# Kernel tuning notes

Hardware: AMD Instinct MI355X
Metric: run time of the kernel (lower is better)

## Reference

```python
import jax, jax.numpy as jnp
import numpy as np

L, D_MODEL, D_INNER, D_STATE, D_CONV, DT_RANK, NUM_ORDERS = 16384, 192, 384, 16, 4, 12, 2
NUM_BLOCKS = 2 * NUM_ORDERS
EPS = 1e-5


def rmsnorm(x, w):
    return x * jax.lax.rsqrt(jnp.mean(x * x, axis=-1, keepdims=True) + EPS) * w


def layernorm(x, w, b):
    m = jnp.mean(x, axis=-1, keepdims=True)
    v = jnp.mean((x - m) ** 2, axis=-1, keepdims=True)
    return (x - m) * jax.lax.rsqrt(v + EPS) * w + b


def causal_dw_conv(x, w, b):
    # x: [L, d], w: [d, K] causal depthwise conv (small fixed K loop)
    K = w.shape[1]
    xp = jnp.pad(x, ((K - 1, 0), (0, 0)))
    y = b
    for k in range(K):
        y = y + xp[k:k + x.shape[0]] * w[:, k]
    return y


def selective_scan(u, dt, A, B, C, Dskip):
    # u, dt: [L, d]; A: [d, n]; B, C: [L, n]; Dskip: [d]
    def step(h, inp):
        u_t, dt_t, B_t, C_t = inp
        dA = jnp.exp(dt_t[:, None] * A)                    # [d, n]
        h = dA * h + (dt_t * u_t)[:, None] * B_t[None, :]  # [d, n]
        return h, h @ C_t                                  # y_t: [d]
    h0 = jnp.zeros(A.shape, u.dtype)
    _, ys = jax.lax.scan(step, h0, (u, dt, B, C))
    return ys + u * Dskip


def mamba_block(x, nw, Wi, cw, cb, Wx, Wdt, bdt, A_log, Dp, Wo):
    # pre-RMSNorm residual Mamba block (create_block semantics)
    res = x
    h = rmsnorm(x, nw)
    xz = h @ Wi                              # [L, 2*d_inner]
    xc, z = jnp.split(xz, 2, axis=-1)
    xc = jax.nn.silu(causal_dw_conv(xc, cw, cb))
    proj = xc @ Wx                           # [L, dt_rank + 2*d_state]
    dt_raw = proj[:, :DT_RANK]
    B = proj[:, DT_RANK:DT_RANK + D_STATE]
    C = proj[:, DT_RANK + D_STATE:]
    dt = jax.nn.softplus(dt_raw @ Wdt + bdt)
    y = selective_scan(xc, dt, -jnp.exp(A_log), B, C, Dp)
    y = y * jax.nn.silu(z)
    return res + y @ Wo


def setup_inputs() -> dict:
    key = jax.random.key(0)
    ks = jax.random.split(key, 10)
    s = 0.02
    x = jax.random.normal(ks[0], (L, D_MODEL), jnp.float32)
    orders = jnp.stack([
        jax.random.permutation(jax.random.fold_in(ks[1], o), L)
        for o in range(NUM_ORDERS)
    ]).astype(jnp.int32)                                     # [NUM_ORDERS, L]
    norm_w = jnp.ones((NUM_BLOCKS, D_MODEL), jnp.float32)
    in_proj_w = jax.random.normal(ks[2], (NUM_BLOCKS, D_MODEL, 2 * D_INNER), jnp.float32) * s
    conv_w = jax.random.normal(ks[3], (NUM_BLOCKS, D_INNER, D_CONV), jnp.float32) * s
    conv_b = jnp.zeros((NUM_BLOCKS, D_INNER), jnp.float32)
    x_proj_w = jax.random.normal(ks[4], (NUM_BLOCKS, D_INNER, DT_RANK + 2 * D_STATE), jnp.float32) * s
    dt_w = jax.random.normal(ks[5], (NUM_BLOCKS, DT_RANK, D_INNER), jnp.float32) * s
    dt_b = jnp.full((NUM_BLOCKS, D_INNER), np.log(np.expm1(0.01)), jnp.float32)  # softplus^-1(0.01)
    A_log = jnp.log(jnp.broadcast_to(jnp.arange(1, D_STATE + 1, dtype=jnp.float32),
                                     (NUM_BLOCKS, D_INNER, D_STATE)))
    D_p = jnp.ones((NUM_BLOCKS, D_INNER), jnp.float32)
    out_proj_w = jax.random.normal(ks[6], (NUM_BLOCKS, D_INNER, D_MODEL), jnp.float32) * s
    fwd_ln_w = jnp.ones((NUM_ORDERS, D_MODEL), jnp.float32)
    fwd_ln_b = jnp.zeros((NUM_ORDERS, D_MODEL), jnp.float32)
    bwd_ln_w = jnp.ones((NUM_ORDERS, D_MODEL), jnp.float32)
    bwd_ln_b = jnp.zeros((NUM_ORDERS, D_MODEL), jnp.float32)
    out_ln_w = jnp.ones((NUM_ORDERS, D_MODEL), jnp.float32)
    out_ln_b = jnp.zeros((NUM_ORDERS, D_MODEL), jnp.float32)
    return {"x": x, "orders": orders, "norm_w": norm_w, "in_proj_w": in_proj_w,
            "conv_w": conv_w, "conv_b": conv_b, "x_proj_w": x_proj_w,
            "dt_w": dt_w, "dt_b": dt_b, "A_log": A_log, "D_p": D_p,
            "out_proj_w": out_proj_w, "fwd_ln_w": fwd_ln_w, "fwd_ln_b": fwd_ln_b,
            "bwd_ln_w": bwd_ln_w, "bwd_ln_b": bwd_ln_b,
            "out_ln_w": out_ln_w, "out_ln_b": out_ln_b}


def reference(x, orders, norm_w, in_proj_w, conv_w, conv_b, x_proj_w, dt_w, dt_b,
              A_log, D_p, out_proj_w, fwd_ln_w, fwd_ln_b, bwd_ln_w, bwd_ln_b,
              out_ln_w, out_ln_b):
    out = x
    for o in range(NUM_ORDERS):          # small fixed loop over serialization orders
        idx = orders[o]
        xo = x[idx]                      # serialize voxel tokens in this order
        fb, bb = o, NUM_ORDERS + o       # forward / backward block indices
        f = mamba_block(xo, norm_w[fb], in_proj_w[fb], conv_w[fb], conv_b[fb],
                        x_proj_w[fb], dt_w[fb], dt_b[fb], A_log[fb], D_p[fb], out_proj_w[fb])
        b = mamba_block(xo[::-1], norm_w[bb], in_proj_w[bb], conv_w[bb], conv_b[bb],
                        x_proj_w[bb], dt_w[bb], dt_b[bb], A_log[bb], D_p[bb], out_proj_w[bb])[::-1]
        comb = layernorm(f, fwd_ln_w[o], fwd_ln_b[o]) + layernorm(b, bwd_ln_w[o], bwd_ln_b[o])
        comb = layernorm(comb, out_ln_w[o], out_ln_b[o])
        out = out + jnp.zeros_like(x).at[idx].set(comb)  # de-serialize (scatter back)
    return out
```

## Files before the change

kernel.cpp:

```cpp
#include <hip/hip_runtime.h>
#include <math.h>

#define LSEQ 16384
#define DM 192
#define DI 384
#define DSN 16
#define DCONV 4
#define DTRK 12
#define NPROJ 44
#define EPSV 1e-5f
#define TCH 32
#define NCH (LSEQ / TCH)
#define GDIM (DI * DSN)
#define RGRP 8
#define NGRP (NCH / RGRP)
#define CT 8


typedef __attribute__((ext_vector_type(8))) short bf16x8;
typedef __attribute__((ext_vector_type(4))) float f32x4;

__device__ __forceinline__ float siluf(float x) { return x / (1.f + __expf(-x)); }
__device__ __forceinline__ float softplus_f(float x) {
  float e = __expf(x);
  float l = __logf(1.f + e);
  return (x > 20.f) ? x : l;
}
__device__ __forceinline__ ushort f2b(float f) {
  uint u = __float_as_uint(f);
  u += 0x7fff + ((u >> 16) & 1);
  return (ushort)(u >> 16);
}
__device__ __forceinline__ float b2f(ushort h) { return __uint_as_float(((uint)h) << 16); }

__device__ __forceinline__ void pow16(float q, float (&a)[16]) {
  float q2 = q*q, q4 = q2*q2, q8 = q4*q4;
  a[0]=q;        a[1]=q2;       a[2]=q2*q;      a[3]=q4;
  a[4]=q4*q;     a[5]=q4*q2;    a[6]=q4*q2*q;   a[7]=q8;
  a[8]=q8*q;     a[9]=q8*q2;    a[10]=q8*q2*q;  a[11]=q8*q4;
  a[12]=q8*q4*q; a[13]=q8*q4*q2;a[14]=q8*q4*q2*q;a[15]=q8*q8;
}

#define PREP_A (4 * 768 * DM)
#define PREP_B (4 * 64 * DI)
#define PREP_C (4 * DM * DI)
__global__ void k_prep(const float* __restrict__ Wi, const float* __restrict__ nw,
                       const float* __restrict__ Wx, const float* __restrict__ Wo,
                       ushort* __restrict__ Wct, ushort* __restrict__ Wxt,
                       ushort* __restrict__ Wot) {
  int i = blockIdx.x * 256 + threadIdx.x;
  if (i < PREP_A) {
    int blk = i / (768 * DM), j = i % (768 * DM);
    int n = j / DM, k = j % DM;
    Wct[i] = f2b(nw[blk*DM + k] * Wi[(size_t)blk*DM*768 + (size_t)k*768 + n]);
  } else if (i < PREP_A + PREP_B) {
    int q = i - PREP_A;
    int blk = q / (64 * DI), j = q % (64 * DI);
    int n = j / DI, k = j % DI;
    Wxt[q] = (n < NPROJ) ? f2b(Wx[(size_t)blk*DI*NPROJ + (size_t)k*NPROJ + n]) : (ushort)0;
  } else if (i < PREP_A + PREP_B + PREP_C) {
    int q = i - PREP_A - PREP_B;
    int blk = q / (DM * DI), j = q % (DM * DI);
    int n = j / DI, k = j % DI;
    Wot[q] = f2b(Wo[(size_t)blk*DI*DM + (size_t)k*DM + n]);
  }
}

__global__ __launch_bounds__(64) void k_gather_rms(const float* __restrict__ x,
                                                   const int* __restrict__ orders,
                                                   ushort* __restrict__ xon) {
  int t = blockIdx.x;
  int o = blockIdx.y;
  int lane = threadIdx.x;
  int r = orders[(size_t)o*LSEQ + t];
  ushort* xo = xon + (size_t)o*LSEQ*DM;
  float v0 = x[(size_t)r*DM + lane];
  float v1 = x[(size_t)r*DM + 64 + lane];
  float v2 = x[(size_t)r*DM + 128 + lane];
  float ss = v0*v0 + v1*v1 + v2*v2;
  #pragma unroll
  for (int oo = 32; oo > 0; oo >>= 1) ss += __shfl_xor(ss, oo);
  float s = rsqrtf(ss * (1.f/DM) + EPSV);
  xo[(size_t)t*DM + lane]       = f2b(v0 * s);
  xo[(size_t)t*DM + 64 + lane]  = f2b(v1 * s);
  xo[(size_t)t*DM + 128 + lane] = f2b(v2 * s);
}

template<int MI, int AMODE, int OMODE>
__global__ __launch_bounds__(256) void k_mm(
    const ushort* __restrict__ A, const ushort* __restrict__ Yp,
    const ushort* __restrict__ Zp, const ushort* __restrict__ Bt,
    void* __restrict__ C0, void* __restrict__ C1,
    int N, int K, int lda, int ldz, int ldc, int aMask,
    long sA, long sY, long sZ, long sB, long sC)
{
  __shared__ __align__(16) ushort As[32 * MI * 64];
  __shared__ __align__(16) ushort Bs[64 * 64];
  const int z = blockIdx.z;
  if (AMODE == 0) A += (size_t)(z & aMask) * sA;
  else { Yp += (size_t)z * sY; Zp += (size_t)z * sZ; }
  Bt += (size_t)z * sB;
  const int bm = blockIdx.x * (32 * MI), bn = blockIdx.y * 64;
  const int tid = threadIdx.x;
  const int l = tid & 63, w = tid >> 6;
  const int wm = w & 1, wn = w >> 1;
  f32x4 acc[MI][2] = {};

  for (int k0 = 0; k0 < K; k0 += 64) {
    #pragma unroll
    for (int p = 0; p < MI; p++) {
      int c = tid + p * 256;
      int row = c >> 3, ko = (c & 7) * 8;
      int sw = (row * 128 + (c & 7) * 16) ^ ((row & 7) << 4);
      if (AMODE == 0) {
        uint4 v = *(const uint4*)(A + (size_t)(bm + row) * lda + k0 + ko);
        *(uint4*)((char*)As + sw) = v;
      } else {
        const ushort* yrow = Yp + (size_t)(bm + row) * lda + k0 + ko;
        const ushort* zrow = Zp + (size_t)(bm + row) * ldz + k0 + ko;
        ushort tmp[8];
        #pragma unroll
        for (int j = 0; j < 8; j++) {
          float zz = b2f(zrow[j]);
          tmp[j] = f2b(b2f(yrow[j]) * (zz / (1.f + __expf(-zz))));
        }
        *(uint4*)((char*)As + sw) = *(const uint4*)tmp;
      }
    }
    #pragma unroll
    for (int p = 0; p < 2; p++) {
      int c = tid + p * 256;
      int row = c >> 3, ko = (c & 7) * 8;
      int sw = (row * 128 + (c & 7) * 16) ^ ((row & 7) << 4);
      uint4 v = *(const uint4*)(Bt + (size_t)(bn + row) * K + k0 + ko);
      *(uint4*)((char*)Bs + sw) = v;
    }
    __syncthreads();
    #pragma unroll
    for (int ks = 0; ks < 2; ks++) {
      bf16x8 af[MI], bfv[2];
      #pragma unroll
      for (int mi = 0; mi < MI; mi++) {
        int r = 16 * MI * wm + 16 * mi + (l & 15);
        int ad = (r * 128 + 32 * ks + 16 * (l >> 4)) ^ ((r & 7) << 4);
        af[mi] = *(const bf16x8*)((const char*)As + ad);
      }
      #pragma unroll
      for (int ni = 0; ni < 2; ni++) {
        int r = 32 * wn + 16 * ni + (l & 15);
        int ad = (r * 128 + 32 * ks + 16 * (l >> 4)) ^ ((r & 7) << 4);
        bfv[ni] = *(const bf16x8*)((const char*)Bs + ad);
      }
      #pragma unroll
      for (int mi = 0; mi < MI; mi++)
        #pragma unroll
        for (int ni = 0; ni < 2; ni++)
          acc[mi][ni] = __builtin_amdgcn_mfma_f32_16x16x32_bf16(
              af[mi], bfv[ni], acc[mi][ni], 0, 0, 0);
    }
    __syncthreads();
  }

  #pragma unroll
  for (int mi = 0; mi < MI; mi++) {
    #pragma unroll
    for (int ni = 0; ni < 2; ni++) {
      int c0 = bn + 32 * wn + 16 * ni + (l & 15);
      if (OMODE != 2 && c0 >= N) continue;
      int r0 = bm + 16 * MI * wm + 16 * mi + 4 * (l >> 4);
      #pragma unroll
      for (int j = 0; j < 4; j++) {
        if (OMODE == 0) {
          ((float*)C0 + (size_t)z*sC)[(size_t)(r0 + j) * ldc + c0] = acc[mi][ni][j];
        } else if (OMODE == 1) {
          ((ushort*)C0 + (size_t)z*sC)[(size_t)(r0 + j) * ldc + c0] = f2b(acc[mi][ni][j]);
        } else {
          if (c0 < 384)
            ((ushort*)C0 + (size_t)z*sC)[(size_t)(r0 + j) * 384 + c0] = f2b(acc[mi][ni][j]);
          else
            ((ushort*)C1 + (size_t)z*sC)[(size_t)(r0 + j) * 384 + (c0 - 384)] = f2b(acc[mi][ni][j]);
        }
      }
    }
  }
}

__global__ __launch_bounds__(256) void k_conv(const ushort* __restrict__ XC,
                                              const float* __restrict__ cw,
                                              const float* __restrict__ cb,
                                              ushort* __restrict__ U) {
  int z = blockIdx.y;
  int blk = z;
  int sgn = 1 - 2*(z >> 1);
  int i = blockIdx.x * 256 + threadIdx.x;
  if (i >= (LSEQ/CT) * (DI/8)) return;
  int tb = i / (DI/8), d0 = (i % (DI/8)) * 8;
  const ushort* X = XC + (size_t)z*LSEQ*DI;
  ushort* Uz = U + (size_t)z*LSEQ*DI;

  float wv[4][8];
  #pragma unroll
  for (int j = 0; j < 8; j++) {
    float4 t4 = *(const float4*)(cw + (size_t)blk*DI*DCONV + (d0+j)*DCONV);
    wv[0][j]=t4.x; wv[1][j]=t4.y; wv[2][j]=t4.z; wv[3][j]=t4.w;
  }
  float cbv[8];
  *(float4*)&cbv[0] = *(const float4*)(cb + blk*DI + d0);
  *(float4*)&cbv[4] = *(const float4*)(cb + blk*DI + d0 + 4);

  int tau0 = tb * CT;
  float win[3][8];
  #pragma unroll
  for (int q = 0; q < 3; q++) {
    int tau = tau0 - 3 + q;
    if (tau >= 0) {
      int r = (sgn > 0) ? tau : (LSEQ-1-tau);
      uint4 xv = *(const uint4*)(X + (size_t)r*DI + d0);
      const ushort* xs = (const ushort*)&xv;
      #pragma unroll
      for (int j = 0; j < 8; j++) win[q][j] = b2f(xs[j]);
    } else {
      #pragma unroll
      for (int j = 0; j < 8; j++) win[q][j] = 0.f;
    }
  }
  #pragma unroll
  for (int tt = 0; tt < CT; tt++) {
    int tau = tau0 + tt;
    int r = (sgn > 0) ? tau : (LSEQ-1-tau);
    float cur[8];
    uint4 xv = *(const uint4*)(X + (size_t)r*DI + d0);
    const ushort* xs = (const ushort*)&xv;
    #pragma unroll
    for (int j = 0; j < 8; j++) cur[j] = b2f(xs[j]);
    ushort outv[8];
    #pragma unroll
    for (int j = 0; j < 8; j++) {
      float a = cbv[j];
      a = fmaf(wv[0][j], win[0][j], a);
      a = fmaf(wv[1][j], win[1][j], a);
      a = fmaf(wv[2][j], win[2][j], a);
      a = fmaf(wv[3][j], cur[j],    a);
      outv[j] = f2b(siluf(a));
    }
    *(uint4*)(Uz + (size_t)r*DI + d0) = *(const uint4*)outv;
    #pragma unroll
    for (int j = 0; j < 8; j++) {
      win[0][j] = win[1][j]; win[1][j] = win[2][j]; win[2][j] = cur[j];
    }
  }
}

__global__ __launch_bounds__(128) void k_scan1(const ushort* __restrict__ UC,
                                               const float* __restrict__ PROJ,
                                               const float* __restrict__ Alog,
                                               const float* __restrict__ Wdt,
                                               const float* __restrict__ bdt,
                                               const float* __restrict__ Dp,
                                               float* __restrict__ Dc,
                                               ushort* __restrict__ Sc,
                                               ushort* __restrict__ Y) {
  __shared__ float Ps[TCH][NPROJ];
  int z = blockIdx.z;
  int blk = z;
  int sgn = 1 - 2*(z >> 1);
  const ushort* Uz = UC + (size_t)z*LSEQ*DI;
  const float* Pz = PROJ + (size_t)z*LSEQ*NPROJ;
  ushort* Yz = Y + (size_t)z*LSEQ*DI;
  int c = blockIdx.y;
  int dd = blockIdx.x * 128;
  int tid = threadIdx.x;
  int d = dd + tid;
  for (int j = tid; j < TCH * 11; j += 128) {
    int row = j / 11, q4 = j % 11;
    int s = c*TCH + row;
    int rg = (sgn > 0) ? s : (LSEQ-1-s);
    *(float4*)&Ps[row][q4*4] = *(const float4*)(Pz + (size_t)rg*NPROJ + q4*4);
  }
  __syncthreads();

  float wdt[DTRK];
  #pragma unroll
  for (int k = 0; k < DTRK; k++) wdt[k] = Wdt[(size_t)blk*DTRK*DI + k*DI + d];
  float bdtv = bdt[blk*DI + d];
  const float* Ablk = Alog + (size_t)blk*GDIM + (size_t)d*DSN;
  bool fast = true;
  #pragma unroll
  for (int n = 0; n < DSN; n++) {
    float An = -__expf(Ablk[n]);
    fast = fast && (fabsf(An + (float)(n+1)) <= 1e-3f * (n+1));
  }
  float dskip = Dp[blk*DI + d];
  float S[DSN] = {};
  float dtsum = 0.f;
  for (int t = 0; t < TCH; t++) {
    int s = c*TCH + t;
    int row = (sgn > 0) ? s : (LSEQ-1-s);
    float u = b2f(Uz[(size_t)row*DI + d]);
    const float* pr = &Ps[t][0];
    float dtp[12], Bv[DSN], Cv[DSN];
    *(float4*)&dtp[0] = *(const float4*)(pr + 0);
    *(float4*)&dtp[4] = *(const float4*)(pr + 4);
    *(float4*)&dtp[8] = *(const float4*)(pr + 8);
    *(float4*)&Bv[0]  = *(const float4*)(pr + 12);
    *(float4*)&Bv[4]  = *(const float4*)(pr + 16);
    *(float4*)&Bv[8]  = *(const float4*)(pr + 20);
    *(float4*)&Bv[12] = *(const float4*)(pr + 24);
    *(float4*)&Cv[0]  = *(const float4*)(pr + 28);
    *(float4*)&Cv[4]  = *(const float4*)(pr + 32);
    *(float4*)&Cv[8]  = *(const float4*)(pr + 36);
    *(float4*)&Cv[12] = *(const float4*)(pr + 40);
    float xdt = bdtv;
    #pragma unroll
    for (int k = 0; k < DTRK; k++) xdt = fmaf(dtp[k], wdt[k], xdt);
    float dtv = softplus_f(xdt);
    float du = dtv * u;
    dtsum += dtv;
    float a[DSN];
    if (fast) { pow16(__expf(-dtv), a); }
    else {
      #pragma unroll
      for (int n = 0; n < DSN; n++) a[n] = __expf(dtv * -__expf(Ablk[n]));
    }
    float y = u * dskip;
    #pragma unroll
    for (int n = 0; n < DSN; n++) {
      S[n] = a[n] * S[n] + du * Bv[n];
      y += S[n] * Cv[n];
    }
    Yz[(size_t)row * DI + d] = f2b(y);
  }
  Dc[(size_t)z*NCH*DI + (size_t)c*DI + d] = dtsum;
  ushort st[16];
  #pragma unroll
  for (int n = 0; n < DSN; n++) st[n] = f2b(S[n]);
  ushort* sp = Sc + (size_t)z*NCH*GDIM + (size_t)c*GDIM + (size_t)d*DSN;
  *(uint4*)sp       = *(const uint4*)&st[0];
  *(uint4*)(sp + 8) = *(const uint4*)&st[8];
}

__global__ __launch_bounds__(256) void k_scan2a(const float* __restrict__ Dc,
                                                const ushort* __restrict__ Sc,
                                                const float* __restrict__ Alog,
                                                float* __restrict__ PL,
                                                float* __restrict__ SL) {
  int g = blockIdx.x * 256 + threadIdx.x;
  int l = blockIdx.y;
  int z = blockIdx.z;
  int blk = z;
  int d = g >> 4;
  float A = -__expf(Alog[(size_t)blk*GDIM + g]);
  const float* Dz = Dc + (size_t)z*NCH*DI;
  const ushort* Sz = Sc + (size_t)z*NCH*GDIM;
  float Da = 0.f, Sa = 0.f;
  #pragma unroll
  for (int j = 0; j < RGRP; j++) {
    int c = l*RGRP + j;
    float D = Dz[(size_t)c*DI + d];
    float p = __expf(A * D);
    Sa = fmaf(p, Sa, b2f(Sz[(size_t)c*GDIM + g]));
    Da += D;
  }
  PL[(size_t)z*NGRP*GDIM + (size_t)l * GDIM + g] = __expf(A * Da);
  SL[(size_t)z*NGRP*GDIM + (size_t)l * GDIM + g] = Sa;
}

__global__ __launch_bounds__(256) void k_scan2b(const float* __restrict__ PL,
                                                const float* __restrict__ SL,
                                                float* __restrict__ HL) {
  int g = blockIdx.x * 256 + threadIdx.x;
  int z = blockIdx.y;
  const float* Pz = PL + (size_t)z*NGRP*GDIM;
  const float* Sz = SL + (size_t)z*NGRP*GDIM;
  float* Hz = HL + (size_t)z*NGRP*GDIM;
  float p[NGRP], s[NGRP];
  #pragma unroll
  for (int l = 0; l < NGRP; l++) {
    p[l] = Pz[(size_t)l * GDIM + g];
    s[l] = Sz[(size_t)l * GDIM + g];
  }
  float H = 0.f;
  #pragma unroll
  for (int l = 0; l < NGRP; l++) {
    Hz[(size_t)l * GDIM + g] = H;
    H = fmaf(p[l], H, s[l]);
  }
}

__global__ __launch_bounds__(256) void k_scan2c(const float* __restrict__ Dc,
                                                const ushort* __restrict__ Sc,
                                                const float* __restrict__ HL,
                                                const float* __restrict__ Alog,
                                                ushort* __restrict__ Hc) {
  int g = blockIdx.x * 256 + threadIdx.x;
  int l = blockIdx.y;
  int z = blockIdx.z;
  int blk = z;
  int d = g >> 4;
  float A = -__expf(Alog[(size_t)blk*GDIM + g]);
  const float* Dz = Dc + (size_t)z*NCH*DI;
  const ushort* Sz = Sc + (size_t)z*NCH*GDIM;
  float h = HL[(size_t)z*NGRP*GDIM + (size_t)l * GDIM + g];
  ushort* Hz = Hc + (size_t)z*NCH*GDIM;
  #pragma unroll
  for (int j = 0; j < RGRP; j++) {
    int c = l*RGRP + j;
    size_t off = (size_t)c * GDIM + g;
    Hz[off] = f2b(h);
    float p = __expf(A * Dz[(size_t)c*DI + d]);
    h = fmaf(p, h, b2f(Sz[off]));
  }
}

__global__ __launch_bounds__(128) void k_fix(const ushort* __restrict__ Hc,
                                             const float* __restrict__ PROJ,
                                             const float* __restrict__ Alog,
                                             const float* __restrict__ Wdt,
                                             const float* __restrict__ bdt,
                                             ushort* __restrict__ Y) {
  __shared__ float Dts[TCH][DTRK];
  __shared__ float Cs[TCH][DSN];
  int z = blockIdx.z;
  int c = blockIdx.y;
  int blk = z;
  int sgn = 1 - 2*(z >> 1);
  int dd = blockIdx.x * 128;
  int tid = threadIdx.x;
  int d = dd + tid;
  const float* Pz = PROJ + (size_t)z*LSEQ*NPROJ;
  ushort* Yz = Y + (size_t)z*LSEQ*DI;

  for (int j = tid; j < TCH * 3; j += 128) {
    int row = j / 3, q4 = j % 3;
    int s = c*TCH + row;
    int rg = (sgn > 0) ? s : (LSEQ-1-s);
    *(float4*)&Dts[row][q4*4] = *(const float4*)(Pz + (size_t)rg*NPROJ + q4*4);
  }
  {
    int row = tid >> 2, q4 = tid & 3;
    int s = c*TCH + row;
    int rg = (sgn > 0) ? s : (LSEQ-1-s);
    *(float4*)&Cs[row][q4*4] = *(const float4*)(Pz + (size_t)rg*NPROJ + 28 + q4*4);
  }

  float wdt[DTRK];
  #pragma unroll
  for (int k = 0; k < DTRK; k++) wdt[k] = Wdt[(size_t)blk*DTRK*DI + k*DI + d];
  float bdtv = bdt[blk*DI + d];
  const float* Ablk = Alog + (size_t)blk*GDIM + (size_t)d*DSN;
  bool fast = true;
  #pragma unroll
  for (int n = 0; n < DSN; n++) {
    float An = -__expf(Ablk[n]);
    fast = fast && (fabsf(An + (float)(n+1)) <= 1e-3f * (n+1));
  }
  float h[DSN];
  {
    const ushort* hp = Hc + (size_t)z*NCH*GDIM + (size_t)c*GDIM + (size_t)d*DSN;
    uint4 h0 = *(const uint4*)hp;
    uint4 h1 = *(const uint4*)(hp + 8);
    const ushort* hs0 = (const ushort*)&h0;
    const ushort* hs1 = (const ushort*)&h1;
    #pragma unroll
    for (int n = 0; n < 8; n++) { h[n] = b2f(hs0[n]); h[8+n] = b2f(hs1[n]); }
  }
  __syncthreads();

  float cd = 0.f;
  for (int t = 0; t < TCH; t++) {
    int s = c*TCH + t;
    int row = (sgn > 0) ? s : (LSEQ-1-s);
    float dtp[12], Cv[DSN];
    *(float4*)&dtp[0] = *(const float4*)&Dts[t][0];
    *(float4*)&dtp[4] = *(const float4*)&Dts[t][4];
    *(float4*)&dtp[8] = *(const float4*)&Dts[t][8];
    *(float4*)&Cv[0]  = *(const float4*)&Cs[t][0];
    *(float4*)&Cv[4]  = *(const float4*)&Cs[t][4];
    *(float4*)&Cv[8]  = *(const float4*)&Cs[t][8];
    *(float4*)&Cv[12] = *(const float4*)&Cs[t][12];
    float xdt = bdtv;
    #pragma unroll
    for (int k = 0; k < DTRK; k++) xdt = fmaf(dtp[k], wdt[k], xdt);
    cd += softplus_f(xdt);
    float p[DSN];
    if (fast) { pow16(__expf(-cd), p); }
    else {
      #pragma unroll
      for (int n = 0; n < DSN; n++) p[n] = __expf(cd * -__expf(Ablk[n]));
    }
    float corr = 0.f;
    #pragma unroll
    for (int n = 0; n < DSN; n++)
      corr = fmaf(p[n] * h[n], Cv[n], corr);
    size_t yi = (size_t)row*DI + d;
    Yz[yi] = f2b(b2f(Yz[yi]) + corr);
  }
}

__device__ __forceinline__ void ln_row(float (&v)[3], const float* __restrict__ w,
                                       const float* __restrict__ b, int lane) {
  float s = v[0] + v[1] + v[2];
  #pragma unroll
  for (int o = 32; o > 0; o >>= 1) s += __shfl_xor(s, o);
  float m = s * (1.f / DM);
  float q = 0.f;
  #pragma unroll
  for (int i = 0; i < 3; i++) { float d = v[i] - m; q += d*d; }
  #pragma unroll
  for (int o = 32; o > 0; o >>= 1) q += __shfl_xor(q, o);
  float inv = rsqrtf(q * (1.f / DM) + EPSV);
  #pragma unroll
  for (int i = 0; i < 3; i++) v[i] = (v[i] - m) * inv * w[lane + 64*i] + b[lane + 64*i];
}

template<int FIRST>
__global__ __launch_bounds__(64) void k_final(const float* __restrict__ x,
                                              const int* __restrict__ idx,
                                              const ushort* __restrict__ G4f,
                                              const ushort* __restrict__ G4b,
                                              const float* __restrict__ lnfw,
                                              const float* __restrict__ lnfb,
                                              const float* __restrict__ lnbw,
                                              const float* __restrict__ lnbb,
                                              const float* __restrict__ lnow,
                                              const float* __restrict__ lnob,
                                              float* __restrict__ out) {
  int t = blockIdx.x, lane = threadIdx.x;
  int r = idx[t];
  float f[3], g[3], cb[3];
  #pragma unroll
  for (int i = 0; i < 3; i++) {
    int j = lane + 64*i;
    float xo = x[(size_t)r*DM + j];
    f[i] = xo + b2f(G4f[(size_t)t*DM + j]);
    g[i] = xo + b2f(G4b[(size_t)t*DM + j]);
  }
  ln_row(f, lnfw, lnfb, lane);
  ln_row(g, lnbw, lnbb, lane);
  #pragma unroll
  for (int i = 0; i < 3; i++) cb[i] = f[i] + g[i];
  ln_row(cb, lnow, lnob, lane);
  #pragma unroll
  for (int i = 0; i < 3; i++) {
    int j = lane + 64*i;
    if (FIRST)
      out[(size_t)r*DM + j] = x[(size_t)r*DM + j] + cb[i];
    else
      out[(size_t)r*DM + j] += cb[i];
  }
}

extern "C" void kernel_launch(void* const* d_in, const int* in_sizes, int n_in,
                              void* d_out, int out_size, void* d_ws, size_t ws_size,
                              hipStream_t stream) {
  const float* x      = (const float*)d_in[0];
  const int*   orders = (const int*)  d_in[1];
  const float* nw     = (const float*)d_in[2];
  const float* Wi     = (const float*)d_in[3];
  const float* cw     = (const float*)d_in[4];
  const float* cbi    = (const float*)d_in[5];
  const float* Wx     = (const float*)d_in[6];
  const float* Wdt    = (const float*)d_in[7];
  const float* bdt    = (const float*)d_in[8];
  const float* Alog   = (const float*)d_in[9];
  const float* Dp     = (const float*)d_in[10];
  const float* Wo     = (const float*)d_in[11];
  const float* flw    = (const float*)d_in[12];
  const float* flb    = (const float*)d_in[13];
  const float* blw    = (const float*)d_in[14];
  const float* blb    = (const float*)d_in[15];
  const float* olw    = (const float*)d_in[16];
  const float* olb    = (const float*)d_in[17];
  float* outp = (float*)d_out;

  char* w = (char*)d_ws;
  size_t off = 0;
  auto take = [&](size_t bytes) -> void* {
    char* p = w + off;
    off += (bytes + 255) & ~(size_t)255;
    return (void*)p;
  };
  ushort* Wct  = (ushort*)take((size_t)4 * 768 * DM * 2);
  ushort* Wxt  = (ushort*)take((size_t)4 * 64 * DI * 2);
  ushort* Wot  = (ushort*)take((size_t)4 * DM * DI * 2);
  ushort* xon  = (ushort*)take((size_t)2 * LSEQ * DM * 2);
  ushort* xc   = (ushort*)take((size_t)4 * LSEQ * DI * 2);
  ushort* zc   = (ushort*)take((size_t)4 * LSEQ * DI * 2);
  ushort* uc   = (ushort*)take((size_t)4 * LSEQ * DI * 2);
  float*  proj = (float*) take((size_t)4 * LSEQ * NPROJ * 4);
  ushort* g4   = (ushort*)take((size_t)4 * LSEQ * DM * 2);
  float*  Dc   = (float*) take((size_t)4 * NCH * DI * 4);
  ushort* Sc   = (ushort*)take((size_t)4 * NCH * GDIM * 2);
  float*  PL   = (float*) take((size_t)4 * NGRP * GDIM * 4);
  float*  SL   = (float*) take((size_t)4 * NGRP * GDIM * 4);
  float*  HL   = (float*) take((size_t)4 * NGRP * GDIM * 4);
  ushort* ybuf = xc;
  ushort* Hc   = uc;
  (void)ws_size; (void)n_in; (void)in_sizes; (void)out_size;

  k_prep<<<(PREP_A + PREP_B + PREP_C + 255)/256, 256, 0, stream>>>(
      Wi, nw, Wx, Wo, Wct, Wxt, Wot);
  k_gather_rms<<<dim3(LSEQ, 2), 64, 0, stream>>>(x, orders, xon);

  k_mm<4,0,2><<<dim3(LSEQ/128, 768/64, 4), 256, 0, stream>>>(
      xon, nullptr, nullptr, Wct, xc, zc, 768, DM, DM, 0, 384, 1,
      (long)LSEQ*DM, 0L, 0L, (long)768*DM, (long)LSEQ*DI);
  k_conv<<<dim3(((LSEQ/CT)*(DI/8) + 255)/256, 4), 256, 0, stream>>>(
      xc, cw, cbi, uc);
  k_mm<2,0,0><<<dim3(LSEQ/64, 1, 4), 256, 0, stream>>>(
      uc, nullptr, nullptr, Wxt, proj, nullptr, NPROJ, DI, DI, 0, NPROJ, 3,
      (long)LSEQ*DI, 0L, 0L, (long)64*DI, (long)LSEQ*NPROJ);
  k_scan1<<<dim3(DI/128, NCH, 4), 128, 0, stream>>>(
      uc, proj, Alog, Wdt, bdt, Dp, Dc, Sc, ybuf);
  k_scan2a<<<dim3(GDIM/256, NGRP, 4), 256, 0, stream>>>(Dc, Sc, Alog, PL, SL);
  k_scan2b<<<dim3(GDIM/256, 4), 256, 0, stream>>>(PL, SL, HL);
  k_scan2c<<<dim3(GDIM/256, NGRP, 4), 256, 0, stream>>>(Dc, Sc, HL, Alog, Hc);
  k_fix<<<dim3(DI/128, NCH, 4), 128, 0, stream>>>(
      Hc, proj, Alog, Wdt, bdt, ybuf);
  k_mm<2,1,1><<<dim3(LSEQ/64, DM/64, 4), 256, 0, stream>>>(
      nullptr, ybuf, zc, Wot, g4, nullptr, DM, DI, DI, DI, DM, 3,
      0L, (long)LSEQ*DI, (long)LSEQ*DI, (long)DM*DI, (long)LSEQ*DM);

  k_final<1><<<LSEQ, 64, 0, stream>>>(x, orders, g4, g4 + (size_t)2*LSEQ*DM,
      flw, flb, blw, blb, olw, olb, outp);
  k_final<0><<<LSEQ, 64, 0, stream>>>(x, orders + LSEQ,
      g4 + (size_t)1*LSEQ*DM, g4 + (size_t)3*LSEQ*DM,
      flw + DM, flb + DM, blw + DM, blb + DM, olw + DM, olb + DM, outp);
}
```

Before: 334.1 us.

## Precompute dt with an MFMA GEMM and store scan carries in bf16

Adds a GEMM that turns the dt_rank slice of proj, written as padded bf16, into softplus(dt) over the full inner dimension, stored as bf16. The scan and fix kernels then load this dt instead of each recomputing a 12-term dot product and softplus. The inter-group scan buffers PL, SL and HL also move from fp32 to bf16 and share a workspace region with the dt_raw buffer. This trades redundant per-element arithmetic for an extra launch plus an extra bf16 tensor of size L×DI per block that must be written and read twice, and it loses some precision in dt and the carried states.

```diff
diff --git a/kernel.cpp b/kernel.cpp
--- a/kernel.cpp
+++ b/kernel.cpp
@@ -44,10 +44,12 @@
 #define PREP_A (4 * 768 * DM)
 #define PREP_B (4 * 64 * DI)
 #define PREP_C (4 * DM * DI)
+#define PREP_D (4 * DI * 64)
 __global__ void k_prep(const float* __restrict__ Wi, const float* __restrict__ nw,
                        const float* __restrict__ Wx, const float* __restrict__ Wo,
+                       const float* __restrict__ Wdt,
                        ushort* __restrict__ Wct, ushort* __restrict__ Wxt,
-                       ushort* __restrict__ Wot) {
+                       ushort* __restrict__ Wot, ushort* __restrict__ Wdtt) {
   int i = blockIdx.x * 256 + threadIdx.x;
   if (i < PREP_A) {
     int blk = i / (768 * DM), j = i % (768 * DM);
@@ -63,6 +65,11 @@
     int blk = q / (DM * DI), j = q % (DM * DI);
     int n = j / DI, k = j % DI;
     Wot[q] = f2b(Wo[(size_t)blk*DI*DM + (size_t)k*DM + n]);
+  } else if (i < PREP_A + PREP_B + PREP_C + PREP_D) {
+    int q = i - PREP_A - PREP_B - PREP_C;
+    int blk = q / (DI * 64), j = q % (DI * 64);
+    int n = j / 64, k = j % 64;
+    Wdtt[q] = (k < DTRK) ? f2b(Wdt[(size_t)blk*DTRK*DI + (size_t)k*DI + n]) : (ushort)0;
   }
 }
 
@@ -90,9 +97,10 @@
 __global__ __launch_bounds__(256) void k_mm(
     const ushort* __restrict__ A, const ushort* __restrict__ Yp,
     const ushort* __restrict__ Zp, const ushort* __restrict__ Bt,
+    const float* __restrict__ bias,
     void* __restrict__ C0, void* __restrict__ C1,
     int N, int K, int lda, int ldz, int ldc, int aMask,
-    long sA, long sY, long sZ, long sB, long sC)
+    long sA, long sY, long sZ, long sB, long sC, long sC1)
 {
   __shared__ __align__(16) ushort As[32 * MI * 64];
   __shared__ __align__(16) ushort Bs[64 * 64];
@@ -166,7 +174,7 @@
     #pragma unroll
     for (int ni = 0; ni < 2; ni++) {
       int c0 = bn + 32 * wn + 16 * ni + (l & 15);
-      if (OMODE != 2 && c0 >= N) continue;
+      if ((OMODE == 0 || OMODE == 1 || OMODE == 4) && c0 >= N) continue;
       int r0 = bm + 16 * MI * wm + 16 * mi + 4 * (l >> 4);
       #pragma unroll
       for (int j = 0; j < 4; j++) {
@@ -174,11 +182,18 @@
           ((float*)C0 + (size_t)z*sC)[(size_t)(r0 + j) * ldc + c0] = acc[mi][ni][j];
         } else if (OMODE == 1) {
           ((ushort*)C0 + (size_t)z*sC)[(size_t)(r0 + j) * ldc + c0] = f2b(acc[mi][ni][j]);
-        } else {
+        } else if (OMODE == 2) {
           if (c0 < 384)
             ((ushort*)C0 + (size_t)z*sC)[(size_t)(r0 + j) * 384 + c0] = f2b(acc[mi][ni][j]);
           else
-            ((ushort*)C1 + (size_t)z*sC)[(size_t)(r0 + j) * 384 + (c0 - 384)] = f2b(acc[mi][ni][j]);
+            ((ushort*)C1 + (size_t)z*sC1)[(size_t)(r0 + j) * 384 + (c0 - 384)] = f2b(acc[mi][ni][j]);
+        } else if (OMODE == 3) {
+          ((ushort*)C1 + (size_t)z*sC1)[(size_t)(r0 + j) * 64 + c0] = f2b(acc[mi][ni][j]);
+          if (c0 < N)
+            ((float*)C0 + (size_t)z*sC)[(size_t)(r0 + j) * ldc + c0] = acc[mi][ni][j];
+        } else {
+          ((ushort*)C0 + (size_t)z*sC)[(size_t)(r0 + j) * ldc + c0] =
+              f2b(softplus_f(acc[mi][ni][j] + bias[(size_t)z*DI + c0]));
         }
       }
     }
@@ -252,37 +267,33 @@
 }
 
 __global__ __launch_bounds__(128) void k_scan1(const ushort* __restrict__ UC,
+                                               const ushort* __restrict__ DT,
                                                const float* __restrict__ PROJ,
                                                const float* __restrict__ Alog,
-                                               const float* __restrict__ Wdt,
-                                               const float* __restrict__ bdt,
                                                const float* __restrict__ Dp,
                                                float* __restrict__ Dc,
                                                ushort* __restrict__ Sc,
                                                ushort* __restrict__ Y) {
-  __shared__ float Ps[TCH][NPROJ];
+  __shared__ float Ps[TCH][32];
   int z = blockIdx.z;
   int blk = z;
   int sgn = 1 - 2*(z >> 1);
   const ushort* Uz = UC + (size_t)z*LSEQ*DI;
+  const ushort* DTz = DT + (size_t)z*LSEQ*DI;
   const float* Pz = PROJ + (size_t)z*LSEQ*NPROJ;
   ushort* Yz = Y + (size_t)z*LSEQ*DI;
   int c = blockIdx.y;
   int dd = blockIdx.x * 128;
   int tid = threadIdx.x;
   int d = dd + tid;
-  for (int j = tid; j < TCH * 11; j += 128) {
-    int row = j / 11, q4 = j % 11;
+  for (int j = tid; j < TCH * 8; j += 128) {
+    int row = j >> 3, q4 = j & 7;
     int s = c*TCH + row;
     int rg = (sgn > 0) ? s : (LSEQ-1-s);
-    *(float4*)&Ps[row][q4*4] = *(const float4*)(Pz + (size_t)rg*NPROJ + q4*4);
+    *(float4*)&Ps[row][q4*4] = *(const float4*)(Pz + (size_t)rg*NPROJ + DTRK + q4*4);
   }
   __syncthreads();
 
-  float wdt[DTRK];
-  #pragma unroll
-  for (int k = 0; k < DTRK; k++) wdt[k] = Wdt[(size_t)blk*DTRK*DI + k*DI + d];
-  float bdtv = bdt[blk*DI + d];
   const float* Ablk = Alog + (size_t)blk*GDIM + (size_t)d*DSN;
   bool fast = true;
   #pragma unroll
@@ -297,23 +308,17 @@
     int s = c*TCH + t;
     int row = (sgn > 0) ? s : (LSEQ-1-s);
     float u = b2f(Uz[(size_t)row*DI + d]);
+    float dtv = b2f(DTz[(size_t)row*DI + d]);
     const float* pr = &Ps[t][0];
-    float dtp[12], Bv[DSN], Cv[DSN];
-    *(float4*)&dtp[0] = *(const float4*)(pr + 0);
-    *(float4*)&dtp[4] = *(const float4*)(pr + 4);
-    *(float4*)&dtp[8] = *(const float4*)(pr + 8);
-    *(float4*)&Bv[0]  = *(const float4*)(pr + 12);
-    *(float4*)&Bv[4]  = *(const float4*)(pr + 16);
-    *(float4*)&Bv[8]  = *(const float4*)(pr + 20);
-    *(float4*)&Bv[12] = *(const float4*)(pr + 24);
-    *(float4*)&Cv[0]  = *(const float4*)(pr + 28);
-    *(float4*)&Cv[4]  = *(const float4*)(pr + 32);
-    *(float4*)&Cv[8]  = *(const float4*)(pr + 36);
-    *(float4*)&Cv[12] = *(const float4*)(pr + 40);
-    float xdt = bdtv;
-    #pragma unroll
-    for (int k = 0; k < DTRK; k++) xdt = fmaf(dtp[k], wdt[k], xdt);
-    float dtv = softplus_f(xdt);
+    float Bv[DSN], Cv[DSN];
+    *(float4*)&Bv[0]  = *(const float4*)(pr + 0);
+    *(float4*)&Bv[4]  = *(const float4*)(pr + 4);
+    *(float4*)&Bv[8]  = *(const float4*)(pr + 8);
+    *(float4*)&Bv[12] = *(const float4*)(pr + 12);
+    *(float4*)&Cv[0]  = *(const float4*)(pr + 16);
+    *(float4*)&Cv[4]  = *(const float4*)(pr + 20);
+    *(float4*)&Cv[8]  = *(const float4*)(pr + 24);
+    *(float4*)&Cv[12] = *(const float4*)(pr + 28);
     float du = dtv * u;
     dtsum += dtv;
     float a[DSN];
@@ -342,8 +347,8 @@
 __global__ __launch_bounds__(256) void k_scan2a(const float* __restrict__ Dc,
                                                 const ushort* __restrict__ Sc,
                                                 const float* __restrict__ Alog,
-                                                float* __restrict__ PL,
-                                                float* __restrict__ SL) {
+                                                ushort* __restrict__ PL,
+                                                ushort* __restrict__ SL) {
   int g = blockIdx.x * 256 + threadIdx.x;
   int l = blockIdx.y;
   int z = blockIdx.z;
@@ -361,35 +366,35 @@
     Sa = fmaf(p, Sa, b2f(Sz[(size_t)c*GDIM + g]));
     Da += D;
   }
-  PL[(size_t)z*NGRP*GDIM + (size_t)l * GDIM + g] = __expf(A * Da);
-  SL[(size_t)z*NGRP*GDIM + (size_t)l * GDIM + g] = Sa;
-}
-
-__global__ __launch_bounds__(256) void k_scan2b(const float* __restrict__ PL,
-                                                const float* __restrict__ SL,
-                                                float* __restrict__ HL) {
+  PL[(size_t)z*NGRP*GDIM + (size_t)l * GDIM + g] = f2b(__expf(A * Da));
+  SL[(size_t)z*NGRP*GDIM + (size_t)l * GDIM + g] = f2b(Sa);
+}
+
+__global__ __launch_bounds__(256) void k_scan2b(const ushort* __restrict__ PL,
+                                                const ushort* __restrict__ SL,
+                                                ushort* __restrict__ HL) {
   int g = blockIdx.x * 256 + threadIdx.x;
   int z = blockIdx.y;
-  const float* Pz = PL + (size_t)z*NGRP*GDIM;
-  const float* Sz = SL + (size_t)z*NGRP*GDIM;
-  float* Hz = HL + (size_t)z*NGRP*GDIM;
+  const ushort* Pz = PL + (size_t)z*NGRP*GDIM;
+  const ushort* Sz = SL + (size_t)z*NGRP*GDIM;
+  ushort* Hz = HL + (size_t)z*NGRP*GDIM;
   float p[NGRP], s[NGRP];
   #pragma unroll
   for (int l = 0; l < NGRP; l++) {
-    p[l] = Pz[(size_t)l * GDIM + g];
-    s[l] = Sz[(size_t)l * GDIM + g];
+    p[l] = b2f(Pz[(size_t)l * GDIM + g]);
+    s[l] = b2f(Sz[(size_t)l * GDIM + g]);
   }
   float H = 0.f;
   #pragma unroll
   for (int l = 0; l < NGRP; l++) {
-    Hz[(size_t)l * GDIM + g] = H;
+    Hz[(size_t)l * GDIM + g] = f2b(H);
     H = fmaf(p[l], H, s[l]);
   }
 }
 
 __global__ __launch_bounds__(256) void k_scan2c(const float* __restrict__ Dc,
                                                 const ushort* __restrict__ Sc,
-                                                const float* __restrict__ HL,
+                                                const ushort* __restrict__ HL,
                                                 const float* __restrict__ Alog,
                                                 ushort* __restrict__ Hc) {
   int g = blockIdx.x * 256 + threadIdx.x;
@@ -400,7 +405,7 @@
   float A = -__expf(Alog[(size_t)blk*GDIM + g]);
   const float* Dz = Dc + (size_t)z*NCH*DI;
   const ushort* Sz = Sc + (size_t)z*NCH*GDIM;
-  float h = HL[(size_t)z*NGRP*GDIM + (size_t)l * GDIM + g];
+  float h = b2f(HL[(size_t)z*NGRP*GDIM + (size_t)l * GDIM + g]);
   ushort* Hz = Hc + (size_t)z*NCH*GDIM;
   #pragma unroll
   for (int j = 0; j < RGRP; j++) {
@@ -413,12 +418,10 @@
 }
 
 __global__ __launch_bounds__(128) void k_fix(const ushort* __restrict__ Hc,
+                                             const ushort* __restrict__ DT,
                                              const float* __restrict__ PROJ,
                                              const float* __restrict__ Alog,
-                                             const float* __restrict__ Wdt,
-                                             const float* __restrict__ bdt,
                                              ushort* __restrict__ Y) {
-  __shared__ float Dts[TCH][DTRK];
   __shared__ float Cs[TCH][DSN];
   int z = blockIdx.z;
   int c = blockIdx.y;
@@ -428,14 +431,9 @@
   int tid = threadIdx.x;
   int d = dd + tid;
   const float* Pz = PROJ + (size_t)z*LSEQ*NPROJ;
+  const ushort* DTz = DT + (size_t)z*LSEQ*DI;
   ushort* Yz = Y + (size_t)z*LSEQ*DI;
 
-  for (int j = tid; j < TCH * 3; j += 128) {
-    int row = j / 3, q4 = j % 3;
-    int s = c*TCH + row;
-    int rg = (sgn > 0) ? s : (LSEQ-1-s);
-    *(float4*)&Dts[row][q4*4] = *(const float4*)(Pz + (size_t)rg*NPROJ + q4*4);
-  }
   {
     int row = tid >> 2, q4 = tid & 3;
     int s = c*TCH + row;
@@ -443,10 +441,6 @@
     *(float4*)&Cs[row][q4*4] = *(const float4*)(Pz + (size_t)rg*NPROJ + 28 + q4*4);
   }
 
-  float wdt[DTRK];
-  #pragma unroll
-  for (int k = 0; k < DTRK; k++) wdt[k] = Wdt[(size_t)blk*DTRK*DI + k*DI + d];
-  float bdtv = bdt[blk*DI + d];
   const float* Ablk = Alog + (size_t)blk*GDIM + (size_t)d*DSN;
   bool fast = true;
   #pragma unroll
@@ -470,24 +464,18 @@
   for (int t = 0; t < TCH; t++) {
     int s = c*TCH + t;
     int row = (sgn > 0) ? s : (LSEQ-1-s);
-    float dtp[12], Cv[DSN];
-    *(float4*)&dtp[0] = *(const float4*)&Dts[t][0];
-    *(float4*)&dtp[4] = *(const float4*)&Dts[t][4];
-    *(float4*)&dtp[8] = *(const float4*)&Dts[t][8];
+    cd += b2f(DTz[(size_t)row*DI + d]);
+    float p[DSN];
+    if (fast) { pow16(__expf(-cd), p); }
+    else {
+      #pragma unroll
+      for (int n = 0; n < DSN; n++) p[n] = __expf(cd * -__expf(Ablk[n]));
+    }
+    float Cv[DSN];
     *(float4*)&Cv[0]  = *(const float4*)&Cs[t][0];
     *(float4*)&Cv[4]  = *(const float4*)&Cs[t][4];
     *(float4*)&Cv[8]  = *(const float4*)&Cs[t][8];
     *(float4*)&Cv[12] = *(const float4*)&Cs[t][12];
-    float xdt = bdtv;
-    #pragma unroll
-    for (int k = 0; k < DTRK; k++) xdt = fmaf(dtp[k], wdt[k], xdt);
-    cd += softplus_f(xdt);
-    float p[DSN];
-    if (fast) { pow16(__expf(-cd), p); }
-    else {
-      #pragma unroll
-      for (int n = 0; n < DSN; n++) p[n] = __expf(cd * -__expf(Ablk[n]));
-    }
     float corr = 0.f;
     #pragma unroll
     for (int n = 0; n < DSN; n++)
@@ -583,43 +571,50 @@
   ushort* Wct  = (ushort*)take((size_t)4 * 768 * DM * 2);
   ushort* Wxt  = (ushort*)take((size_t)4 * 64 * DI * 2);
   ushort* Wot  = (ushort*)take((size_t)4 * DM * DI * 2);
+  ushort* Wdtt = (ushort*)take((size_t)4 * DI * 64 * 2);
   ushort* xon  = (ushort*)take((size_t)2 * LSEQ * DM * 2);
   ushort* xc   = (ushort*)take((size_t)4 * LSEQ * DI * 2);
   ushort* zc   = (ushort*)take((size_t)4 * LSEQ * DI * 2);
   ushort* uc   = (ushort*)take((size_t)4 * LSEQ * DI * 2);
   float*  proj = (float*) take((size_t)4 * LSEQ * NPROJ * 4);
-  ushort* g4   = (ushort*)take((size_t)4 * LSEQ * DM * 2);
   float*  Dc   = (float*) take((size_t)4 * NCH * DI * 4);
   ushort* Sc   = (ushort*)take((size_t)4 * NCH * GDIM * 2);
-  float*  PL   = (float*) take((size_t)4 * NGRP * GDIM * 4);
-  float*  SL   = (float*) take((size_t)4 * NGRP * GDIM * 4);
-  float*  HL   = (float*) take((size_t)4 * NGRP * GDIM * 4);
+  ushort* DTb  = (ushort*)take((size_t)4 * LSEQ * DI * 2);
+  ushort* reg  = (ushort*)take((size_t)3 * 4 * NGRP * GDIM * 2);
+  ushort* dtraw= reg;
+  ushort* PL   = reg;
+  ushort* SL   = reg + (size_t)4 * NGRP * GDIM;
+  ushort* HL   = reg + (size_t)8 * NGRP * GDIM;
   ushort* ybuf = xc;
   ushort* Hc   = uc;
+  ushort* g4   = DTb;
   (void)ws_size; (void)n_in; (void)in_sizes; (void)out_size;
 
-  k_prep<<<(PREP_A + PREP_B + PREP_C + 255)/256, 256, 0, stream>>>(
-      Wi, nw, Wx, Wo, Wct, Wxt, Wot);
+  k_prep<<<(PREP_A + PREP_B + PREP_C + PREP_D + 255)/256, 256, 0, stream>>>(
+      Wi, nw, Wx, Wo, Wdt, Wct, Wxt, Wot, Wdtt);
   k_gather_rms<<<dim3(LSEQ, 2), 64, 0, stream>>>(x, orders, xon);
 
   k_mm<4,0,2><<<dim3(LSEQ/128, 768/64, 4), 256, 0, stream>>>(
-      xon, nullptr, nullptr, Wct, xc, zc, 768, DM, DM, 0, 384, 1,
-      (long)LSEQ*DM, 0L, 0L, (long)768*DM, (long)LSEQ*DI);
+      xon, nullptr, nullptr, Wct, nullptr, xc, zc, 768, DM, DM, 0, 384, 1,
+      (long)LSEQ*DM, 0L, 0L, (long)768*DM, (long)LSEQ*DI, (long)LSEQ*DI);
   k_conv<<<dim3(((LSEQ/CT)*(DI/8) + 255)/256, 4), 256, 0, stream>>>(
       xc, cw, cbi, uc);
-  k_mm<2,0,0><<<dim3(LSEQ/64, 1, 4), 256, 0, stream>>>(
-      uc, nullptr, nullptr, Wxt, proj, nullptr, NPROJ, DI, DI, 0, NPROJ, 3,
-      (long)LSEQ*DI, 0L, 0L, (long)64*DI, (long)LSEQ*NPROJ);
+  k_mm<2,0,3><<<dim3(LSEQ/64, 1, 4), 256, 0, stream>>>(
+      uc, nullptr, nullptr, Wxt, nullptr, proj, dtraw, NPROJ, DI, DI, 0, NPROJ, 3,
+      (long)LSEQ*DI, 0L, 0L, (long)64*DI, (long)LSEQ*NPROJ, (long)LSEQ*64);
+  k_mm<2,0,4><<<dim3(LSEQ/64, DI/64, 4), 256, 0, stream>>>(
+      dtraw, nullptr, nullptr, Wdtt, bdt, DTb, nullptr, DI, 64, 64, 0, DI, 3,
+      (long)LSEQ*64, 0L, 0L, (long)DI*64, (long)LSEQ*DI, 0L);
   k_scan1<<<dim3(DI/128, NCH, 4), 128, 0, stream>>>(
-      uc, proj, Alog, Wdt, bdt, Dp, Dc, Sc, ybuf);
+      uc, DTb, proj, Alog, Dp, Dc, Sc, ybuf);
   k_scan2a<<<dim3(GDIM/256, NGRP, 4), 256, 0, stream>>>(Dc, Sc, Alog, PL, SL);
   k_scan2b<<<dim3(GDIM/256, 4), 256, 0, stream>>>(PL, SL, HL);
   k_scan2c<<<dim3(GDIM/256, NGRP, 4), 256, 0, stream>>>(Dc, Sc, HL, Alog, Hc);
   k_fix<<<dim3(DI/128, NCH, 4), 128, 0, stream>>>(
-      Hc, proj, Alog, Wdt, bdt, ybuf);
+      Hc, DTb, proj, Alog, ybuf);
   k_mm<2,1,1><<<dim3(LSEQ/64, DM/64, 4), 256, 0, stream>>>(
-      nullptr, ybuf, zc, Wot, g4, nullptr, DM, DI, DI, DI, DM, 3,
-      0L, (long)LSEQ*DI, (long)LSEQ*DI, (long)DM*DI, (long)LSEQ*DM);
+      nullptr, ybuf, zc, Wot, nullptr, g4, nullptr, DM, DI, DI, DI, DM, 3,
+      0L, (long)LSEQ*DI, (long)LSEQ*DI, (long)DM*DI, (long)LSEQ*DM, 0L);
 
   k_final<1><<<LSEQ, 64, 0, stream>>>(x, orders, g4, g4 + (size_t)2*LSEQ*DM,
       flw, flb, blw, blb, olw, olb, outp);
```

Measured after the change: 353.3 us. 5.7% more time.
